# Kernel optimization log

Hardware: AMD Instinct MI355X
Metric: run time of the kernel (lower is better)

The kernel has to match this reference:

```python
import jax, jax.numpy as jnp
import numpy as np

N_NODES = 512
HEADS = 4
CO = 64        # per-head out channels (PyG GATConv out_channels)
NEG_SLOPE = 0.2  # PyG GATConv default negative_slope


def setup_inputs() -> dict:
    key = jax.random.key(0)
    k0, k1, k2, k3, k4 = jax.random.split(key, 5)
    B, C, T, N = 8, 64, 12, N_NODES
    E = 8192
    x = jax.random.normal(k0, (B, C, T, N), dtype=jnp.float32)
    edge_index = jax.random.randint(k1, (2, E), 0, N, dtype=jnp.int32)
    # learned params of GATConv(in=64, out=64, heads=4, concat=False)
    W = jax.random.normal(k2, (C, HEADS * CO), dtype=jnp.float32) / np.sqrt(C).astype(np.float32)
    att_src = jax.random.normal(k3, (HEADS, CO), dtype=jnp.float32) * 0.1
    att_dst = jax.random.normal(k4, (HEADS, CO), dtype=jnp.float32) * 0.1
    bias = jnp.zeros((CO,), dtype=jnp.float32)
    return {"x": x, "edge_index": edge_index, "W": W,
            "att_src": att_src, "att_dst": att_dst, "bias": bias}


def reference(x, edge_index, W, att_src, att_dst, bias):
    # x: [B, C, T, N] -> batch of G = B*T graphs, all sharing edge_index.
    B, C, T, N = x.shape
    H, Co = att_src.shape
    G = B * T
    xg = x.transpose(0, 2, 3, 1).reshape(G, N, C)              # [G,N,C]
    h = (xg @ W).reshape(G, N, H, Co)                          # [G,N,H,Co]
    a_src = jnp.einsum('gnhc,hc->gnh', h, att_src)             # [G,N,H]
    a_dst = jnp.einsum('gnhc,hc->gnh', h, att_dst)             # [G,N,H]
    # add self loops (PyG GATConv default)
    loops = jnp.arange(N, dtype=edge_index.dtype)
    src = jnp.concatenate([edge_index[0], loops])              # [E']
    dst = jnp.concatenate([edge_index[1], loops])              # [E']
    # attention logits per edge, leading edge axis for segment ops
    logits = jax.nn.leaky_relu(a_src[:, src] + a_dst[:, dst], NEG_SLOPE)  # [G,E',H]
    logits = logits.transpose(1, 0, 2)                         # [E',G,H]
    m = jax.ops.segment_max(logits, dst, num_segments=N)       # [N,G,H]
    e = jnp.exp(logits - m[dst])
    s = jax.ops.segment_sum(e, dst, num_segments=N)            # [N,G,H]
    alpha = e / s[dst]                                         # [E',G,H]  (dropout off: eval)
    msg = alpha[..., None] * h[:, src].transpose(1, 0, 2, 3)   # [E',G,H,Co]
    out = jax.ops.segment_sum(msg, dst, num_segments=N)        # [N,G,H,Co]
    out = out.mean(axis=2) + bias                              # [N,G,Co]  concat=False -> head mean
    out = out.transpose(1, 0, 2).reshape(B, T, N, Co)          # [B,T,N,Co]
    return out.transpose(0, 3, 1, 2)                           # [B,Co,T,N]
```

## Files before the change

kernel.cpp:

```cpp
#include <hip/hip_runtime.h>

#define B_  8
#define C_  64
#define T_  12
#define N_  512
#define E_  8192
#define H_  4
#define CO_ 64
#define G_  (B_ * T_)
#define EP_ (E_ + N_)
#define MAXDEG 128
#define POISON 0xAAAAAAAAu

typedef __bf16 bf16x8 __attribute__((ext_vector_type(8)));
typedef unsigned short usx8 __attribute__((ext_vector_type(8)));
typedef float  f32x4  __attribute__((ext_vector_type(4)));

static __device__ __forceinline__ unsigned short f2bf(float f) {
    unsigned int u = __float_as_uint(f);
    return (unsigned short)((u + 0x7fffu + ((u >> 16) & 1u)) >> 16);
}

__global__ __launch_bounds__(256) void k_prep(
    const float* __restrict__ x, const int* __restrict__ ei,
    const float* __restrict__ W,
    const float* __restrict__ att_src, const float* __restrict__ att_dst,
    unsigned short* __restrict__ xtb, float* __restrict__ as_, float* __restrict__ ad_,
    unsigned int* __restrict__ cnt, int* __restrict__ srclist,
    unsigned short* __restrict__ Wfrag)
{
    int bid = blockIdx.x, tid = threadIdx.x;

    if (bid >= 768) {
        if (bid < 800) {
            int e = (bid - 768) * 256 + tid;
            int d = ei[E_ + e], s = ei[e];
            unsigned int pos = atomicAdd(&cnt[d], 1u) - POISON;
            srclist[d * MAXDEG + pos] = s;
        } else {
            int base = (bid - 800) * 2048;
            #pragma unroll
            for (int it = 0; it < 8; ++it) {
                int idx = base + it * 256 + tid;
                int c  = idx >> 8, r = idx & 255;
                int hh = r >> 6,  co = r & 63;
                int k  = hh * 64 + c;
                int ks = k >> 5, kq = (k >> 3) & 3, j = k & 7;
                int nt = co >> 4, l = kq * 16 + (co & 15);
                Wfrag[(size_t)((ks * 4 + nt) * 64 + l) * 8 + j] = f2bf(W[idx]);
            }
        }
        return;
    }

    __shared__ float xs[64][65];
    __shared__ float Wls[64][4], Wld[64][4];
    __shared__ float sa[64][5], sd[64][5];

    int lane = tid & 63, q = tid >> 6;

    {
        const float4* W4 = reinterpret_cast<const float4*>(W);
        const float4* A4 = reinterpret_cast<const float4*>(att_src);
        const float4* D4 = reinterpret_cast<const float4*>(att_dst);
        float4 uu = A4[lane];
        float4 vv = D4[lane];
        #pragma unroll
        for (int it = 0; it < 16; ++it) {
            int idx4 = tid + it * 256;
            float4 w = W4[idx4];
            float s1 = w.x*uu.x + w.y*uu.y + w.z*uu.z + w.w*uu.w;
            float s2 = w.x*vv.x + w.y*vv.y + w.z*vv.z + w.w*vv.w;
            #pragma unroll
            for (int off = 1; off < 16; off <<= 1) {
                s1 += __shfl_xor(s1, off, 64);
                s2 += __shfl_xor(s2, off, 64);
            }
            if ((lane & 15) == 0) {
                Wls[q + it * 4][lane >> 4] = s1;
                Wld[q + it * 4][lane >> 4] = s2;
            }
        }
    }

    int g  = bid >> 3, tl = bid & 7;
    int b  = g / T_, t = g - b * T_;
    int n0 = tl * 64;

    #pragma unroll
    for (int i = 0; i < 16; ++i) {
        int c = q + i * 4;
        xs[c][lane] = x[((size_t)(b * C_ + c) * T_ + t) * N_ + n0 + lane];
    }
    __syncthreads();

    float s1 = 0.f, s2 = 0.f;
    for (int c = 0; c < 64; ++c) {
        float v = xs[c][lane];
        s1 += v * Wls[c][q];
        s2 += v * Wld[c][q];
    }
    sa[lane][q] = s1;
    sd[lane][q] = s2;

    #pragma unroll
    for (int i = 0; i < 16; ++i) {
        int nl = q + i * 4;
        xtb[((size_t)(g * N_ + n0 + nl)) * 64 + lane] = f2bf(xs[lane][nl]);
    }
    __syncthreads();

    int nl = tid >> 2, hh = tid & 3;
    as_[((size_t)(g * N_ + n0 + nl)) * 4 + hh] = sa[nl][hh];
    ad_[((size_t)(g * N_ + n0 + nl)) * 4 + hh] = sd[nl][hh];
}

__global__ __launch_bounds__(256) void k_fused(
    const unsigned short* __restrict__ xtb, const float* __restrict__ as_,
    const float* __restrict__ ad_,
    const unsigned int* __restrict__ cnt, const int* __restrict__ srclist,
    const unsigned short* __restrict__ Wfrag, const float* __restrict__ bias,
    float* __restrict__ out)
{
    __shared__ __align__(16) char lds[53248];
    float* wb  = reinterpret_cast<float*>(lds + 32768);
    int*   ss  = reinterpret_cast<int*>(lds + 49152);
    float (*tl)[65] = reinterpret_cast<float (*)[65]>(lds + 32768);

    int bid  = blockIdx.x;
    int xcd  = bid & 7, rest = bid >> 3;
    int gq   = rest % 12, tile = rest / 12;
    int g    = xcd * 12 + gq;
    int n0   = tile * 64;
    int b    = g / T_, t = g - b * T_;
    int tid  = threadIdx.x;
    int wave = tid >> 6, lane = tid & 63;

    int u    = lane >> 5;
    int slot = wave * 2 + u;
    int ch2  = (lane & 31) * 2;
    const unsigned short* xg = xtb + ((size_t)g * N_) * 64 + ch2;

    int fslot = tid >> 5;
    int fhh   = tid & 3;
    int fp    = (tid >> 2) & 7;
    int fe    = tid & 31;

    for (int pass = 0; pass < 8; ++pass) {
        int nb = n0 + pass * 8;

        {
            int node = nb + fslot;
            int dgS  = (int)(cnt[node] - POISON);
            int dgP  = (int)(cnt[nb + (fslot ^ 1)] - POISON);
            int dtf  = max(dgS, dgP) + 1;
            float adv = ad_[((size_t)(g * N_ + node)) * 4 + fhh];
            for (int e = fp; e < dgS; e += 8) {
                int s = srclist[node * MAXDEG + e];
                float v = as_[((size_t)(g * N_ + s)) * 4 + fhh] + adv;
                v = v > 0.f ? v : 0.2f * v;
                wb[((fslot * MAXDEG) + e) * 4 + fhh] = __expf(v);
            }
            if (fp == 0) {
                float v = as_[((size_t)(g * N_ + node)) * 4 + fhh] + adv;
                v = v > 0.f ? v : 0.2f * v;
                wb[((fslot * MAXDEG) + dgS) * 4 + fhh] = __expf(v);
            }
            for (int e = dgS + 1 + fp; e < dtf; e += 8)
                wb[((fslot * MAXDEG) + e) * 4 + fhh] = 0.f;
            for (int e = fe; e < dtf; e += 32)
                ss[fslot * MAXDEG + e] = (e < dgS) ? srclist[node * MAXDEG + e] : node;
        }
        __syncthreads();

        int dgA  = (int)(cnt[nb + wave * 2]     - POISON);
        int dgB  = (int)(cnt[nb + wave * 2 + 1] - POISON);
        int dtot = max(dgA, dgB) + 1;
        const int*   sbase = ss + slot * MAXDEG;
        const float* wbase = wb + slot * MAXDEG * 4;

        float zA0=0.f, zA1=0.f, zA2=0.f, zA3=0.f;
        float zB0=0.f, zB1=0.f, zB2=0.f, zB3=0.f;
        float s0=0.f, s1=0.f, s2=0.f, s3=0.f;
        int e = 0;
        for (; e + 8 <= dtot; e += 8) {
            unsigned int xv[8];
            #pragma unroll
            for (int j = 0; j < 8; ++j)
                xv[j] = *reinterpret_cast<const unsigned int*>(xg + (size_t)sbase[e + j] * 64);
            #pragma unroll
            for (int j = 0; j < 8; ++j) {
                float x0 = __uint_as_float(xv[j] << 16);
                float x1 = __uint_as_float(xv[j] & 0xffff0000u);
                float4 w = *reinterpret_cast<const float4*>(wbase + (e + j) * 4);
                zA0 += w.x * x0;  zB0 += w.x * x1;  s0 += w.x;
                zA1 += w.y * x0;  zB1 += w.y * x1;  s1 += w.y;
                zA2 += w.z * x0;  zB2 += w.z * x1;  s2 += w.z;
                zA3 += w.w * x0;  zB3 += w.w * x1;  s3 += w.w;
            }
        }
        for (; e < dtot; ++e) {
            unsigned int xv = *reinterpret_cast<const unsigned int*>(xg + (size_t)sbase[e] * 64);
            float x0 = __uint_as_float(xv << 16);
            float x1 = __uint_as_float(xv & 0xffff0000u);
            float4 w = *reinterpret_cast<const float4*>(wbase + e * 4);
            zA0 += w.x * x0;  zB0 += w.x * x1;  s0 += w.x;
            zA1 += w.y * x0;  zB1 += w.y * x1;  s1 += w.y;
            zA2 += w.z * x0;  zB2 += w.z * x1;  s2 += w.z;
            zA3 += w.w * x0;  zB3 += w.w * x1;  s3 += w.w;
        }

        int nl = pass * 8 + slot;
        unsigned int sw  = (unsigned int)((nl & 7) << 4);
        unsigned int o0  = (unsigned int)(nl * 512 + ch2 * 2);
        unsigned int p0 = (unsigned int)f2bf(zA0 / s0) | ((unsigned int)f2bf(zB0 / s0) << 16);
        unsigned int p1 = (unsigned int)f2bf(zA1 / s1) | ((unsigned int)f2bf(zB1 / s1) << 16);
        unsigned int p2 = (unsigned int)f2bf(zA2 / s2) | ((unsigned int)f2bf(zB2 / s2) << 16);
        unsigned int p3 = (unsigned int)f2bf(zA3 / s3) | ((unsigned int)f2bf(zB3 / s3) << 16);
        *reinterpret_cast<unsigned int*>(lds + ((o0 +   0) ^ sw)) = p0;
        *reinterpret_cast<unsigned int*>(lds + ((o0 + 128) ^ sw)) = p1;
        *reinterpret_cast<unsigned int*>(lds + ((o0 + 256) ^ sw)) = p2;
        *reinterpret_cast<unsigned int*>(lds + ((o0 + 384) ^ sw)) = p3;
        __syncthreads();
    }

    int m = lane & 15, quad = lane >> 4;
    int nrow = wave * 16 + m;
    unsigned int swr = (unsigned int)((m & 7) << 4);

    f32x4 acc[4];
    #pragma unroll
    for (int nt = 0; nt < 4; ++nt) acc[nt] = (f32x4){0.f, 0.f, 0.f, 0.f};

    #pragma unroll
    for (int ks = 0; ks < 8; ++ks) {
        unsigned int ro = (unsigned int)(nrow * 512 + quad * 16 + ks * 64);
        uint4 za = *reinterpret_cast<const uint4*>(lds + (ro ^ swr));
        bf16x8 a = __builtin_bit_cast(bf16x8, za);
        #pragma unroll
        for (int nt = 0; nt < 4; ++nt) {
            usx8 ub = *reinterpret_cast<const usx8*>(
                Wfrag + (size_t)(((ks * 4 + nt) * 64 + lane) * 8));
            bf16x8 bw = __builtin_bit_cast(bf16x8, ub);
            acc[nt] = __builtin_amdgcn_mfma_f32_16x16x32_bf16(a, bw, acc[nt], 0, 0, 0);
        }
    }

    #pragma unroll
    for (int nt = 0; nt < 4; ++nt) {
        int co = nt * 16 + m;
        float bv = bias[co];
        #pragma unroll
        for (int rr = 0; rr < 4; ++rr) {
            int row = wave * 16 + quad * 4 + rr;
            tl[row][co] = 0.25f * acc[nt][rr] + bv;
        }
    }
    __syncthreads();

    #pragma unroll
    for (int it = 0; it < 16; ++it) {
        int c = wave + it * 4;
        out[((size_t)(b * CO_ + c) * T_ + t) * N_ + n0 + lane] = tl[lane][c];
    }
}

extern "C" void kernel_launch(void* const* d_in, const int* in_sizes, int n_in,
                              void* d_out, int out_size, void* d_ws, size_t ws_size,
                              hipStream_t stream) {
    const float* x       = (const float*)d_in[0];
    const int*   ei      = (const int*)  d_in[1];
    const float* W       = (const float*)d_in[2];
    const float* att_src = (const float*)d_in[3];
    const float* att_dst = (const float*)d_in[4];
    const float* bias    = (const float*)d_in[5];
    float* out = (float*)d_out;

    char* p = (char*)d_ws;
    unsigned short* xtb = (unsigned short*)p; p += (size_t)G_ * N_ * C_ * sizeof(unsigned short);
    float* as_     = (float*)p;  p += (size_t)G_ * N_ * H_ * sizeof(float);
    float* ad_     = (float*)p;  p += (size_t)G_ * N_ * H_ * sizeof(float);
    unsigned short* Wfrag = (unsigned short*)p; p += 64 * 256 * sizeof(unsigned short);
    unsigned int* cnt = (unsigned int*)p; p += 512 * sizeof(unsigned int);
    int* srclist   = (int*)p;    p += N_ * MAXDEG * sizeof(int);

    k_prep  <<<808, 256, 0, stream>>>(x, ei, W, att_src, att_dst,
                                      xtb, as_, ad_, cnt, srclist, Wfrag);
    k_fused <<<768, 256, 0, stream>>>(xtb, as_, ad_, cnt, srclist, Wfrag, bias, out);
}
```

Before: 124.8 us.

## Compute edge attention weights per half-wave and broadcast via ds_bpermute, dropping barriers

Each half-wave now owns one destination node at a time. Its 32 lanes compute the leaky-relu/exp edge weights and source indices for up to 32 edges in registers, then broadcast them to the whole half-wave with ds_bpermute during aggregation. This removes the block-wide LDS staging of weights and source lists and the two __syncthreads per pass. It also shrinks LDS from about 52KB to 32KB, which can raise occupancy. The cost is five bpermutes per edge in the inner loop, and a loop bound that is dynamic per wave rather than a fixed unroll.

```diff
diff --git a/kernel.cpp b/kernel.cpp
--- a/kernel.cpp
+++ b/kernel.cpp
@@ -122,10 +122,8 @@
     const unsigned short* __restrict__ Wfrag, const float* __restrict__ bias,
     float* __restrict__ out)
 {
-    __shared__ __align__(16) char lds[53248];
-    float* wb  = reinterpret_cast<float*>(lds + 32768);
-    int*   ss  = reinterpret_cast<int*>(lds + 49152);
-    float (*tl)[65] = reinterpret_cast<float (*)[65]>(lds + 32768);
+    __shared__ __align__(16) char lds[32768];
+    float (*tl)[65] = reinterpret_cast<float (*)[65]>(lds);
 
     int bid  = blockIdx.x;
     int xcd  = bid & 7, rest = bid >> 3;
@@ -135,82 +133,63 @@
     int b    = g / T_, t = g - b * T_;
     int tid  = threadIdx.x;
     int wave = tid >> 6, lane = tid & 63;
-
-    int u    = lane >> 5;
-    int slot = wave * 2 + u;
-    int ch2  = (lane & 31) * 2;
+    int hw   = tid >> 5;
+    int hl   = lane & 31;
+    int ch2  = hl * 2;
+
     const unsigned short* xg = xtb + ((size_t)g * N_) * 64 + ch2;
-
-    int fslot = tid >> 5;
-    int fhh   = tid & 3;
-    int fp    = (tid >> 2) & 7;
-    int fe    = tid & 31;
-
-    for (int pass = 0; pass < 8; ++pass) {
-        int nb = n0 + pass * 8;
-
-        {
-            int node = nb + fslot;
-            int dgS  = (int)(cnt[node] - POISON);
-            int dgP  = (int)(cnt[nb + (fslot ^ 1)] - POISON);
-            int dtf  = max(dgS, dgP) + 1;
-            float adv = ad_[((size_t)(g * N_ + node)) * 4 + fhh];
-            for (int e = fp; e < dgS; e += 8) {
-                int s = srclist[node * MAXDEG + e];
-                float v = as_[((size_t)(g * N_ + s)) * 4 + fhh] + adv;
-                v = v > 0.f ? v : 0.2f * v;
-                wb[((fslot * MAXDEG) + e) * 4 + fhh] = __expf(v);
-            }
-            if (fp == 0) {
-                float v = as_[((size_t)(g * N_ + node)) * 4 + fhh] + adv;
-                v = v > 0.f ? v : 0.2f * v;
-                wb[((fslot * MAXDEG) + dgS) * 4 + fhh] = __expf(v);
-            }
-            for (int e = dgS + 1 + fp; e < dtf; e += 8)
-                wb[((fslot * MAXDEG) + e) * 4 + fhh] = 0.f;
-            for (int e = fe; e < dtf; e += 32)
-                ss[fslot * MAXDEG + e] = (e < dgS) ? srclist[node * MAXDEG + e] : node;
-        }
-        __syncthreads();
-
-        int dgA  = (int)(cnt[nb + wave * 2]     - POISON);
-        int dgB  = (int)(cnt[nb + wave * 2 + 1] - POISON);
-        int dtot = max(dgA, dgB) + 1;
-        const int*   sbase = ss + slot * MAXDEG;
-        const float* wbase = wb + slot * MAXDEG * 4;
+    const float4* as4 = reinterpret_cast<const float4*>(as_) + (size_t)g * N_;
+    const float4* ad4 = reinterpret_cast<const float4*>(ad_) + (size_t)g * N_;
+    int permbase = (lane & 32) << 2;
+
+    for (int k = 0; k < 8; ++k) {
+        int node = n0 + hw * 8 + k;
+        int dg   = (int)(cnt[node] - POISON);
+        int dt   = dg + 1;
+        int dtmax = max(dt, __shfl_xor(dt, 32, 64));
+        dtmax = __builtin_amdgcn_readfirstlane(dtmax);
+        float4 adv = ad4[node];
+        const int* srow = srclist + node * MAXDEG;
 
         float zA0=0.f, zA1=0.f, zA2=0.f, zA3=0.f;
         float zB0=0.f, zB1=0.f, zB2=0.f, zB3=0.f;
         float s0=0.f, s1=0.f, s2=0.f, s3=0.f;
-        int e = 0;
-        for (; e + 8 <= dtot; e += 8) {
-            unsigned int xv[8];
-            #pragma unroll
-            for (int j = 0; j < 8; ++j)
-                xv[j] = *reinterpret_cast<const unsigned int*>(xg + (size_t)sbase[e + j] * 64);
-            #pragma unroll
-            for (int j = 0; j < 8; ++j) {
-                float x0 = __uint_as_float(xv[j] << 16);
-                float x1 = __uint_as_float(xv[j] & 0xffff0000u);
-                float4 w = *reinterpret_cast<const float4*>(wbase + (e + j) * 4);
-                zA0 += w.x * x0;  zB0 += w.x * x1;  s0 += w.x;
-                zA1 += w.y * x0;  zB1 += w.y * x1;  s1 += w.y;
-                zA2 += w.z * x0;  zB2 += w.z * x1;  s2 += w.z;
-                zA3 += w.w * x0;  zB3 += w.w * x1;  s3 += w.w;
-            }
-        }
-        for (; e < dtot; ++e) {
-            unsigned int xv = *reinterpret_cast<const unsigned int*>(xg + (size_t)sbase[e] * 64);
-            float x0 = __uint_as_float(xv << 16);
-            float x1 = __uint_as_float(xv & 0xffff0000u);
-            float4 w = *reinterpret_cast<const float4*>(wbase + e * 4);
-            zA0 += w.x * x0;  zB0 += w.x * x1;  s0 += w.x;
-            zA1 += w.y * x0;  zB1 += w.y * x1;  s1 += w.y;
-            zA2 += w.z * x0;  zB2 += w.z * x1;  s2 += w.z;
-            zA3 += w.w * x0;  zB3 += w.w * x1;  s3 += w.w;
-        }
-
-        int nl = pass * 8 + slot;
+
+        for (int c0 = 0; c0 < dtmax; c0 += 32) {
+            int e   = c0 + hl;
+            int sw_ = node;
+            if (e < dg) sw_ = srow[e];
+            float4 av = as4[sw_];
+            float v0 = av.x + adv.x; v0 = v0 > 0.f ? v0 : 0.2f * v0;
+            float v1 = av.y + adv.y; v1 = v1 > 0.f ? v1 : 0.2f * v1;
+            float v2 = av.z + adv.z; v2 = v2 > 0.f ? v2 : 0.2f * v2;
+            float v3 = av.w + adv.w; v3 = v3 > 0.f ? v3 : 0.2f * v3;
+            bool live = (e <= dg);
+            int w0i = live ? __float_as_int(__expf(v0)) : 0;
+            int w1i = live ? __float_as_int(__expf(v1)) : 0;
+            int w2i = live ? __float_as_int(__expf(v2)) : 0;
+            int w3i = live ? __float_as_int(__expf(v3)) : 0;
+
+            int jcnt = min(32, dtmax - c0);
+            #pragma unroll 8
+            for (int j = 0; j < jcnt; ++j) {
+                int addr = permbase + (j << 2);
+                int si   = __builtin_amdgcn_ds_bpermute(addr, sw_);
+                float wa = __int_as_float(__builtin_amdgcn_ds_bpermute(addr, w0i));
+                float wb = __int_as_float(__builtin_amdgcn_ds_bpermute(addr, w1i));
+                float wc = __int_as_float(__builtin_amdgcn_ds_bpermute(addr, w2i));
+                float wd = __int_as_float(__builtin_amdgcn_ds_bpermute(addr, w3i));
+                unsigned int xv = *reinterpret_cast<const unsigned int*>(xg + (size_t)si * 64);
+                float x0 = __uint_as_float(xv << 16);
+                float x1 = __uint_as_float(xv & 0xffff0000u);
+                zA0 += wa * x0;  zB0 += wa * x1;  s0 += wa;
+                zA1 += wb * x0;  zB1 += wb * x1;  s1 += wb;
+                zA2 += wc * x0;  zB2 += wc * x1;  s2 += wc;
+                zA3 += wd * x0;  zB3 += wd * x1;  s3 += wd;
+            }
+        }
+
+        int nl = hw * 8 + k;
         unsigned int sw  = (unsigned int)((nl & 7) << 4);
         unsigned int o0  = (unsigned int)(nl * 512 + ch2 * 2);
         unsigned int p0 = (unsigned int)f2bf(zA0 / s0) | ((unsigned int)f2bf(zB0 / s0) << 16);
@@ -221,7 +200,6 @@
         *reinterpret_cast<unsigned int*>(lds + ((o0 + 128) ^ sw)) = p1;
         *reinterpret_cast<unsigned int*>(lds + ((o0 + 256) ^ sw)) = p2;
         *reinterpret_cast<unsigned int*>(lds + ((o0 + 384) ^ sw)) = p3;
-        __syncthreads();
     }
 
     int m = lane & 15, quad = lane >> 4;
@@ -245,6 +223,7 @@
             acc[nt] = __builtin_amdgcn_mfma_f32_16x16x32_bf16(a, bw, acc[nt], 0, 0, 0);
         }
     }
+    __syncthreads();
 
     #pragma unroll
     for (int nt = 0; nt < 4; ++nt) {
```

Result: slower. 132.1 us (+5.8%).
